# Optimization experiments

Hardware: AMD Instinct MI355X
Metric: run time of the kernel (lower is better)

Reference implementation:

```python
import jax, jax.numpy as jnp
import numpy as np

STRIDE, PAD, DIL, K = 1, 1, 1, 3  # spatial conv hyperparams (temporal kernel = 1)


def setup_inputs() -> dict:
    key = jax.random.key(0)
    k0, k1, k2, k3 = jax.random.split(key, 4)
    C_in, C_out = 256, 256
    x = jax.random.normal(k0, (2, C_in, 8, 32, 32), jnp.float32)
    # main weight keeps the dummy temporal dim of size 1, as in the torch module
    weight = jax.random.normal(k1, (C_out, C_in, 1, K, K), jnp.float32) * 0.02
    bias = jnp.zeros((C_out,), jnp.float32)
    # conv_offset: 27 = 2*9 offsets + 9 masks (3x3 kernel, 1 deformable group).
    # torch inits these to zero; use small random values so sampling is non-trivial.
    offset_w = jax.random.normal(k2, (27, C_in, 3, 3), jnp.float32) * 0.01
    offset_b = jax.random.normal(k3, (27,), jnp.float32) * 0.01
    return {"x": x, "weight": weight, "bias": bias,
            "offset_w": offset_w, "offset_b": offset_b}


def _dcn_forward(x, weight, bias, offset_w, offset_b):
    B, C, T, H, W = x.shape
    N = B * T
    # (B,C,T,H,W) -> (B*T, C, H, W)
    xf = x.transpose(0, 2, 1, 3, 4).reshape(N, C, H, W)

    # offset/mask conv (standard 3x3 conv, padding=dilation)
    om = jax.lax.conv_general_dilated(
        xf, offset_w, (STRIDE, STRIDE), [(PAD, PAD), (PAD, PAD)],
        rhs_dilation=(DIL, DIL), dimension_numbers=("NCHW", "OIHW", "NCHW"))
    om = om + offset_b[None, :, None, None]
    o1, o2, mask = jnp.split(om, 3, axis=1)              # each [N,9,Ho,Wo]
    offset = jnp.concatenate([o1, o2], axis=1)           # [N,18,Ho,Wo]
    mask = jax.nn.sigmoid(mask)
    Ho, Wo = om.shape[2], om.shape[3]
    KK = K * K

    # DCNv2 layout: interleaved (dy, dx) pairs per kernel tap
    off = offset.reshape(N, KK, 2, Ho, Wo)
    dy, dx = off[:, :, 0], off[:, :, 1]                  # [N,9,Ho,Wo]

    ki = jnp.arange(KK) // K
    kj = jnp.arange(KK) % K
    base_y = (jnp.arange(Ho) * STRIDE - PAD)[None, :] + (ki * DIL)[:, None]  # [9,Ho]
    base_x = (jnp.arange(Wo) * STRIDE - PAD)[None, :] + (kj * DIL)[:, None]  # [9,Wo]
    py = dy + base_y[None, :, :, None].astype(dy.dtype)  # [N,9,Ho,Wo]
    px = dx + base_x[None, :, None, :].astype(dx.dtype)

    y0f = jnp.floor(py); x0f = jnp.floor(px)
    ty = py - y0f; tx = px - x0f
    y0 = y0f.astype(jnp.int32); x0 = x0f.astype(jnp.int32)

    x_flat = xf.reshape(N, C, H * W)

    def gather(yy, xx, w):
        # zero padding outside image; bilinear corner weight w: [N,9,Ho,Wo]
        valid = (yy >= 0) & (yy < H) & (xx >= 0) & (xx < W)
        idx = (jnp.clip(yy, 0, H - 1) * W + jnp.clip(xx, 0, W - 1)).reshape(N, -1)
        v = jnp.take_along_axis(x_flat, idx[:, None, :], axis=2)   # [N,C,9*Ho*Wo]
        return v * (w * valid).reshape(N, 1, -1)

    val = (gather(y0,     x0,     (1 - ty) * (1 - tx))
           + gather(y0,     x0 + 1, (1 - ty) * tx)
           + gather(y0 + 1, x0,     ty * (1 - tx))
           + gather(y0 + 1, x0 + 1, ty * tx))
    val = val.reshape(N, C, KK, Ho, Wo) * mask[:, None]            # modulated samples

    w2 = weight.squeeze(2).reshape(weight.shape[0], C, KK)         # [Co,C,9]
    out = jnp.einsum('nckhw,ock->nohw', val, w2) + bias[None, :, None, None]
    # (B*T, Co, Ho, Wo) -> (B, Co, T, Ho, Wo)
    return out.reshape(B, T, -1, Ho, Wo).transpose(0, 2, 1, 3, 4)


def reference(x, weight, bias, offset_w, offset_b):
    return _dcn_forward(x, weight, bias, offset_w, offset_b)
```

## Files before the change

### kernel.cpp

```cpp
#include <hip/hip_runtime.h>
#include <math.h>

typedef __attribute__((ext_vector_type(4))) float f32x4;
typedef __attribute__((ext_vector_type(2))) float f32x2;
typedef __attribute__((ext_vector_type(8))) short s16x8;

__device__ inline unsigned f2bf(float f) {
    unsigned u = __float_as_uint(f);
    u += 0x7FFFu + ((u >> 16) & 1u);
    return u >> 16;
}
__device__ inline f32x2 unpk2(unsigned u) {
    f32x2 r;
    r.x = __uint_as_float(u << 16);
    r.y = __uint_as_float(u & 0xFFFF0000u);
    return r;
}

__global__ __launch_bounds__(256) void pack_all(const float* __restrict__ x,
                                                const float* __restrict__ w,
                                                const float* __restrict__ ow,
                                                unsigned* __restrict__ xt32,
                                                short* __restrict__ Wp,
                                                short* __restrict__ Wo)
{
    __shared__ float tile[256][33];
    const int tid = threadIdx.x;
    if (blockIdx.x < 512) {
        const int n = blockIdx.x >> 5, y = blockIdx.x & 31;
        const int b = n >> 3, ts = n & 7;
        const float* src = x + (((size_t)b * 256 * 8) + ts) * 1024 + y * 32;
        #pragma unroll
        for (int rep = 0; rep < 32; ++rep) {
            int c = rep * 8 + (tid >> 5);
            int ww = tid & 31;
            tile[c][ww] = src[(size_t)c * 8192 + ww];
        }
        __syncthreads();
        unsigned* dst = xt32 + ((size_t)n * 1024 + y * 32) * 128;
        #pragma unroll
        for (int rep = 0; rep < 16; ++rep) {
            int idx = rep * 256 + tid;
            int cp = idx & 127, ww = idx >> 7;
            unsigned lo = f2bf(tile[2 * cp][ww]);
            unsigned hi = f2bf(tile[2 * cp + 1][ww]);
            dst[(size_t)ww * 128 + cp] = lo | (hi << 16);
        }
    } else if (blockIdx.x < 768) {
        const int o = blockIdx.x - 512;
        float* lw = &tile[0][0];
        for (int k = tid; k < 2304; k += 256) lw[k] = w[(size_t)o * 2304 + k];
        __syncthreads();
        const int oq = o >> 6, mt = (o >> 4) & 3, l15 = o & 15;
        for (int idx = tid; idx < 288; idx += 256) {
            int t = idx >> 5, cb = idx & 31;
            int quad = cb & 3, kc = (cb >> 2) & 1, k2 = cb >> 3;
            int lane = quad * 16 + l15;
            union { s16x8 v; short sh[8]; } u;
            #pragma unroll
            for (int c8 = 0; c8 < 8; ++c8)
                u.sh[c8] = (short)f2bf(lw[(cb * 8 + c8) * 9 + t]);
            size_t dst = ((((size_t)(t * 4 + oq) * 4 + mt) * 4 + k2) * 2 + kc) * 512
                       + lane * 8;
            *(s16x8*)(Wp + dst) = u.v;
        }
    } else {
        const int m = blockIdx.x - 768;
        float* lw = &tile[0][0];
        if (m < 27) {
            for (int k = tid; k < 2304; k += 256) lw[k] = ow[(size_t)m * 2304 + k];
        }
        __syncthreads();
        #pragma unroll
        for (int t = 0; t < 9; ++t) {
            float v = (m < 27) ? lw[tid * 9 + t] : 0.f;
            Wo[t * 8192 + m * 256 + tid] = (short)f2bf(v);
        }
    }
}

__global__ __launch_bounds__(512) void offsets_kernel(
    const short* __restrict__ xt, const short* __restrict__ Wo,
    const float* __restrict__ ob, float4* __restrict__ descW,
    int4* __restrict__ descI)
{
    __shared__ float pom[4][32][33];
    const int tid = threadIdx.x;
    const int bs = blockIdx.x;
    const int n = bs >> 5, ho = bs & 31;
    const int lane = tid & 63, wv = tid >> 6;
    const int nt = wv & 1, kq4 = wv >> 1;
    const int l15 = lane & 15, quad = lane >> 4;
    const int pos = nt * 16 + l15;
    const short* xn = xt + (size_t)n * (1024 * 256);
    const s16x8 z8 = {0, 0, 0, 0, 0, 0, 0, 0};

    f32x4 oacc0 = {0, 0, 0, 0}, oacc1 = {0, 0, 0, 0};
    #pragma unroll
    for (int t = 0; t < 9; ++t) {
        const int ki = t / 3, kj = t - 3 * ki;
        int y = ho - 1 + ki;
        bool vy = (y >= 0) && (y < 32);
        int ycl = min(max(y, 0), 31);
        int xc = pos - 1 + kj;
        bool v = vy && (xc >= 0) && (xc < 32);
        int xcl = min(max(xc, 0), 31);
        const short* bp  = xn + (ycl * 32 + xcl) * 256;
        const short* ap0 = Wo + (t * 32 + l15) * 256;
        #pragma unroll
        for (int cc = 0; cc < 2; ++cc) {
            int c = kq4 * 64 + cc * 32 + quad * 8;
            s16x8 bfrag = *(const s16x8*)(bp + c);
            if (!v) bfrag = z8;
            s16x8 a0 = *(const s16x8*)(ap0 + c);
            s16x8 a1 = *(const s16x8*)(ap0 + 16 * 256 + c);
            oacc0 = __builtin_amdgcn_mfma_f32_16x16x32_bf16(a0, bfrag, oacc0, 0, 0, 0);
            oacc1 = __builtin_amdgcn_mfma_f32_16x16x32_bf16(a1, bfrag, oacc1, 0, 0, 0);
        }
    }
    #pragma unroll
    for (int r = 0; r < 4; ++r) {
        pom[kq4][quad * 4 + r][pos]      = oacc0[r];
        pom[kq4][16 + quad * 4 + r][pos] = oacc1[r];
    }
    __syncthreads();

    for (int s = tid; s < 288; s += 512) {
        int t = s >> 5, wo = s & 31;
        float dy = pom[0][2 * t][wo]     + pom[1][2 * t][wo]
                 + pom[2][2 * t][wo]     + pom[3][2 * t][wo]     + ob[2 * t];
        float dx = pom[0][2 * t + 1][wo] + pom[1][2 * t + 1][wo]
                 + pom[2][2 * t + 1][wo] + pom[3][2 * t + 1][wo] + ob[2 * t + 1];
        float mv = pom[0][18 + t][wo]    + pom[1][18 + t][wo]
                 + pom[2][18 + t][wo]    + pom[3][18 + t][wo]    + ob[18 + t];
        float mk = 1.0f / (1.0f + __expf(-mv));
        float py = dy + (float)(ho - 1 + t / 3);
        float px = dx + (float)(wo - 1 + t % 3);
        float y0f = floorf(py), x0f = floorf(px);
        float ty = py - y0f, tx = px - x0f;
        int y0 = (int)y0f, x0 = (int)x0f;
        int y1 = y0 + 1, x1 = x0 + 1;
        bool vy0 = (y0 >= 0) && (y0 < 32), vy1 = (y1 >= 0) && (y1 < 32);
        bool vx0 = (x0 >= 0) && (x0 < 32), vx1 = (x1 >= 0) && (x1 < 32);
        int cy0 = min(max(y0, 0), 31), cy1 = min(max(y1, 0), 31);
        int cx0 = min(max(x0, 0), 31), cx1 = min(max(x1, 0), 31);
        float b0 = (1.f - ty) * (1.f - tx) * mk * (float)(vy0 && vx0);
        float b1 = (1.f - ty) * tx         * mk * (float)(vy0 && vx1);
        float b2 = ty * (1.f - tx)         * mk * (float)(vy1 && vx0);
        float b3 = ty * tx                 * mk * (float)(vy1 && vx1);
        size_t base = (size_t)(n * 32 + ho) * 288 + s;
        descW[base] = make_float4(b0, b1, b2, b3);
        descI[base] = make_int4((cy0 * 32 + cx0) * 256, (cy0 * 32 + cx1) * 256,
                                (cy1 * 32 + cx0) * 256, (cy1 * 32 + cx1) * 256);
    }
}

template<int NK>
__global__ __launch_bounds__(256, 4) void dcn_main(
    const short* __restrict__ xt, const short* __restrict__ Wp,
    const float4* __restrict__ descW, const int4* __restrict__ descI,
    const float* __restrict__ bias, float* __restrict__ out,
    float* __restrict__ wsP)
{
    __shared__ short  sB[2][32 * 72];
    __shared__ float4 sdw[288];
    __shared__ int4   sdi[288];

    const int tid = threadIdx.x;
    constexpr int NQ = 4 / NK;
    const int bid0 = blockIdx.x;
    const int bid = (bid0 & 7) * (64 * NQ) + (bid0 >> 3);
    const int kq = bid & (NQ - 1);
    const int r  = bid / NQ;
    const int n = r >> 5, ho = r & 31;

    {
        const float4* dW = descW + (size_t)(n * 32 + ho) * 288;
        const int4*   dI = descI + (size_t)(n * 32 + ho) * 288;
        for (int i = tid; i < 288; i += 256) { sdw[i] = dW[i]; sdi[i] = dI[i]; }
    }
    __syncthreads();

    const int oct = tid & 7, pos = tid >> 3;
    const int oq = tid >> 6;
    const int lane = tid & 63, l15 = lane & 15, quad = lane >> 4;
    const short* xn = xt + (size_t)n * (1024 * 256);

    f32x4 acc[8];
    #pragma unroll
    for (int i = 0; i < 8; ++i) acc[i] = (f32x4){0, 0, 0, 0};

    uint4  g[2][4];
    float4 gw[2];

    {
        gw[0] = sdw[pos];
        const int4 i4 = sdi[pos];
        const int cc = (kq * NK) * 64 + oct * 8;
        g[0][0] = *(const uint4*)(xn + i4.x + cc);
        g[0][1] = *(const uint4*)(xn + i4.y + cc);
        g[0][2] = *(const uint4*)(xn + i4.z + cc);
        g[0][3] = *(const uint4*)(xn + i4.w + cc);
    }

    #pragma unroll
    for (int s = 0; s < 9 * NK; ++s) {
        const int cur = s & 1, nxt = cur ^ 1;
        const int t = s % 9;
        const int k2 = kq * NK + s / 9;

        s16x8 afr[4][2];
        #pragma unroll
        for (int mt = 0; mt < 4; ++mt)
            #pragma unroll
            for (int kc = 0; kc < 2; ++kc)
                afr[mt][kc] = *(const s16x8*)(Wp +
                    ((((size_t)(t * 4 + oq) * 4 + mt) * 4 + k2) * 2 + kc) * 512
                    + lane * 8);

        {
            const float4 w4 = gw[cur];
            const unsigned* p0 = (const unsigned*)&g[cur][0];
            const unsigned* p1 = (const unsigned*)&g[cur][1];
            const unsigned* p2 = (const unsigned*)&g[cur][2];
            const unsigned* p3 = (const unsigned*)&g[cur][3];
            union { s16x8 v; unsigned u[4]; } bu;
            #pragma unroll
            for (int d = 0; d < 4; ++d) {
                f32x2 a = w4.x * unpk2(p0[d]);
                a += w4.y * unpk2(p1[d]);
                a += w4.z * unpk2(p2[d]);
                a += w4.w * unpk2(p3[d]);
                asm("v_cvt_pk_bf16_f32 %0, %1, %2"
                    : "=v"(bu.u[d]) : "v"(a.x), "v"(a.y));
            }
            *(s16x8*)&sB[cur][pos * 72 + oct * 8] = bu.v;
        }

        asm volatile("s_waitcnt lgkmcnt(0)\n\ts_barrier" ::: "memory");
        __builtin_amdgcn_sched_barrier(0);

        if (s < 9 * NK - 1) {
            const int t1 = (s + 1) % 9;
            const int cb1 = (kq * NK + (s + 1) / 9) * 64;
            gw[nxt] = sdw[t1 * 32 + pos];
            const int4 i4 = sdi[t1 * 32 + pos];
            const int cc = cb1 + oct * 8;
            g[nxt][0] = *(const uint4*)(xn + i4.x + cc);
            g[nxt][1] = *(const uint4*)(xn + i4.y + cc);
            g[nxt][2] = *(const uint4*)(xn + i4.z + cc);
            g[nxt][3] = *(const uint4*)(xn + i4.w + cc);
        }

        s16x8 bfr[2][2];
        #pragma unroll
        for (int nt = 0; nt < 2; ++nt)
            #pragma unroll
            for (int kc = 0; kc < 2; ++kc)
                bfr[nt][kc] = *(const s16x8*)
                    &sB[cur][(nt * 16 + l15) * 72 + kc * 32 + quad * 8];

        #pragma unroll
        for (int mt = 0; mt < 4; ++mt)
            #pragma unroll
            for (int nt = 0; nt < 2; ++nt) {
                acc[mt * 2 + nt] = __builtin_amdgcn_mfma_f32_16x16x32_bf16(
                    afr[mt][0], bfr[nt][0], acc[mt * 2 + nt], 0, 0, 0);
                acc[mt * 2 + nt] = __builtin_amdgcn_mfma_f32_16x16x32_bf16(
                    afr[mt][1], bfr[nt][1], acc[mt * 2 + nt], 0, 0, 0);
            }
    }

    const int bb = n >> 3, ts = n & 7;
    if (kq == 0) {
        #pragma unroll
        for (int mt = 0; mt < 4; ++mt) {
            const float4 bv = *(const float4*)(bias + oq * 64 + mt * 16 + quad * 4);
            #pragma unroll
            for (int nt = 0; nt < 2; ++nt)
                #pragma unroll
                for (int rr = 0; rr < 4; ++rr) {
                    int oc = oq * 64 + mt * 16 + quad * 4 + rr;
                    int p  = nt * 16 + l15;
                    out[(((size_t)bb * 256 + oc) * 8 + ts) * 1024 + ho * 32 + p] =
                        acc[mt * 2 + nt][rr] + ((const float*)&bv)[rr];
                }
        }
    } else {
        float* wp1 = wsP + (size_t)(kq - 1) * 4194304
                         + (size_t)(n * 32 + ho) * 256 * 32;
        #pragma unroll
        for (int mt = 0; mt < 4; ++mt)
            #pragma unroll
            for (int nt = 0; nt < 2; ++nt)
                #pragma unroll
                for (int rr = 0; rr < 4; ++rr) {
                    int oc = oq * 64 + mt * 16 + quad * 4 + rr;
                    int p  = nt * 16 + l15;
                    wp1[oc * 32 + p] = acc[mt * 2 + nt][rr];
                }
    }
}

template<int NP>
__global__ __launch_bounds__(256) void reduce_out(const float* __restrict__ wsP,
                                                  float4* __restrict__ out)
{
    int i = blockIdx.x * 256 + threadIdx.x;
    int f = i * 4;
    int p  = f & 1023;
    int ts = (f >> 10) & 7;
    int oc = (f >> 13) & 255;
    int bb = f >> 21;
    int n = bb * 8 + ts;
    int ho = p >> 5, pp = p & 31;
    size_t base = ((size_t)(n * 32 + ho) * 256 + oc) * 32 + pp;
    float4 a = out[i];
    #pragma unroll
    for (int q = 0; q < NP; ++q) {
        const float4 w = *(const float4*)(wsP + (size_t)q * 4194304 + base);
        a.x += w.x; a.y += w.y; a.z += w.z; a.w += w.w;
    }
    out[i] = a;
}

extern "C" void kernel_launch(void* const* d_in, const int* in_sizes, int n_in,
                              void* d_out, int out_size, void* d_ws, size_t ws_size,
                              hipStream_t stream) {
    const float* x        = (const float*)d_in[0];
    const float* weight   = (const float*)d_in[1];
    const float* bias     = (const float*)d_in[2];
    const float* offset_w = (const float*)d_in[3];
    const float* offset_b = (const float*)d_in[4];

    char* ws = (char*)d_ws;
    short*  xt    = (short*)ws;                       ws += (size_t)16 * 1024 * 256 * 2;
    short*  Wp    = (short*)ws;                       ws += (size_t)9 * 256 * 256 * 2;
    short*  Wo    = (short*)ws;                       ws += (size_t)9 * 32 * 256 * 2;
    float4* descW = (float4*)ws;                      ws += (size_t)147456 * 16;
    int4*   descI = (int4*)ws;                        ws += (size_t)147456 * 16;
    float*  wsP   = (float*)ws;

    const bool big = ws_size >= 64765952ULL;

    pack_all      <<<800,  256, 0, stream>>>(x, weight, offset_w, (unsigned*)xt, Wp, Wo);
    offsets_kernel<<<512,  512, 0, stream>>>(xt, Wo, offset_b, descW, descI);
    if (big) {
        dcn_main<1>   <<<2048, 256, 0, stream>>>(xt, Wp, descW, descI, bias, (float*)d_out, wsP);
        reduce_out<3> <<<4096, 256, 0, stream>>>(wsP, (float4*)d_out);
    } else {
        dcn_main<2>   <<<1024, 256, 0, stream>>>(xt, Wp, descW, descI, bias, (float*)d_out, wsP);
        reduce_out<1> <<<4096, 256, 0, stream>>>(wsP, (float4*)d_out);
    }
}
```

Before: 153.0 us.

## Replace split-K DCN main kernel plus reduction with single full-K block kernel

The main deformable-conv GEMM no longer splits the 256 input channels across several blocks that write partial sums to a workspace. One 512-thread block now covers all channels for an output row, two 128-channel halves per tap, and writes the biased output directly. This drops the reduce_out kernel launch and the workspace write/read traffic. In exchange there are fewer blocks (512) for the GPU to spread over, a longer serial loop per block, and each bilinear sample is gathered only once per row.

```diff
diff --git a/kernel.cpp b/kernel.cpp
--- a/kernel.cpp
+++ b/kernel.cpp
@@ -155,40 +155,36 @@
     }
 }
 
-template<int NK>
-__global__ __launch_bounds__(256, 4) void dcn_main(
+__global__ __launch_bounds__(512, 4) void dcn_single(
     const short* __restrict__ xt, const short* __restrict__ Wp,
     const float4* __restrict__ descW, const int4* __restrict__ descI,
-    const float* __restrict__ bias, float* __restrict__ out,
-    float* __restrict__ wsP)
+    const float* __restrict__ bias, float* __restrict__ out)
 {
-    __shared__ short  sB[2][32 * 72];
+    __shared__ short  sB[2][32 * 136];
     __shared__ float4 sdw[288];
     __shared__ int4   sdi[288];
 
     const int tid = threadIdx.x;
-    constexpr int NQ = 4 / NK;
     const int bid0 = blockIdx.x;
-    const int bid = (bid0 & 7) * (64 * NQ) + (bid0 >> 3);
-    const int kq = bid & (NQ - 1);
-    const int r  = bid / NQ;
-    const int n = r >> 5, ho = r & 31;
+    const int bid = (bid0 & 7) * 64 + (bid0 >> 3);
+    const int n = bid >> 5, ho = bid & 31;
 
     {
         const float4* dW = descW + (size_t)(n * 32 + ho) * 288;
         const int4*   dI = descI + (size_t)(n * 32 + ho) * 288;
-        for (int i = tid; i < 288; i += 256) { sdw[i] = dW[i]; sdi[i] = dI[i]; }
+        for (int i = tid; i < 288; i += 512) { sdw[i] = dW[i]; sdi[i] = dI[i]; }
     }
     __syncthreads();
 
-    const int oct = tid & 7, pos = tid >> 3;
-    const int oq = tid >> 6;
+    const int oct16 = tid & 15, pos = tid >> 4;
+    const int wv = tid >> 6;
+    const int oq = wv >> 1, mtb = (wv & 1) * 2;
     const int lane = tid & 63, l15 = lane & 15, quad = lane >> 4;
     const short* xn = xt + (size_t)n * (1024 * 256);
 
-    f32x4 acc[8];
-    #pragma unroll
-    for (int i = 0; i < 8; ++i) acc[i] = (f32x4){0, 0, 0, 0};
+    f32x4 acc[4];
+    #pragma unroll
+    for (int i = 0; i < 4; ++i) acc[i] = (f32x4){0, 0, 0, 0};
 
     uint4  g[2][4];
     float4 gw[2];
@@ -196,7 +192,7 @@
     {
         gw[0] = sdw[pos];
         const int4 i4 = sdi[pos];
-        const int cc = (kq * NK) * 64 + oct * 8;
+        const int cc = oct16 * 8;
         g[0][0] = *(const uint4*)(xn + i4.x + cc);
         g[0][1] = *(const uint4*)(xn + i4.y + cc);
         g[0][2] = *(const uint4*)(xn + i4.z + cc);
@@ -204,19 +200,21 @@
     }
 
     #pragma unroll
-    for (int s = 0; s < 9 * NK; ++s) {
+    for (int s = 0; s < 18; ++s) {
         const int cur = s & 1, nxt = cur ^ 1;
         const int t = s % 9;
-        const int k2 = kq * NK + s / 9;
-
-        s16x8 afr[4][2];
-        #pragma unroll
-        for (int mt = 0; mt < 4; ++mt)
-            #pragma unroll
-            for (int kc = 0; kc < 2; ++kc)
-                afr[mt][kc] = *(const s16x8*)(Wp +
-                    ((((size_t)(t * 4 + oq) * 4 + mt) * 4 + k2) * 2 + kc) * 512
+        const int h = s / 9;
+
+        s16x8 afr[2][4];
+        #pragma unroll
+        for (int mt = 0; mt < 2; ++mt)
+            #pragma unroll
+            for (int kp = 0; kp < 4; ++kp) {
+                const int k2 = h * 2 + (kp >> 1), kc = kp & 1;
+                afr[mt][kp] = *(const s16x8*)(Wp +
+                    ((((size_t)(t * 4 + oq) * 4 + (mtb + mt)) * 4 + k2) * 2 + kc) * 512
                     + lane * 8);
+            }
 
         {
             const float4 w4 = gw[cur];
@@ -234,94 +232,56 @@
                 asm("v_cvt_pk_bf16_f32 %0, %1, %2"
                     : "=v"(bu.u[d]) : "v"(a.x), "v"(a.y));
             }
-            *(s16x8*)&sB[cur][pos * 72 + oct * 8] = bu.v;
+            *(s16x8*)&sB[cur][pos * 136 + oct16 * 8] = bu.v;
         }
 
         asm volatile("s_waitcnt lgkmcnt(0)\n\ts_barrier" ::: "memory");
         __builtin_amdgcn_sched_barrier(0);
 
-        if (s < 9 * NK - 1) {
+        if (s < 17) {
             const int t1 = (s + 1) % 9;
-            const int cb1 = (kq * NK + (s + 1) / 9) * 64;
+            const int h1 = (s + 1) / 9;
             gw[nxt] = sdw[t1 * 32 + pos];
             const int4 i4 = sdi[t1 * 32 + pos];
-            const int cc = cb1 + oct * 8;
+            const int cc = h1 * 128 + oct16 * 8;
             g[nxt][0] = *(const uint4*)(xn + i4.x + cc);
             g[nxt][1] = *(const uint4*)(xn + i4.y + cc);
             g[nxt][2] = *(const uint4*)(xn + i4.z + cc);
             g[nxt][3] = *(const uint4*)(xn + i4.w + cc);
         }
 
-        s16x8 bfr[2][2];
+        s16x8 bfr[2][4];
         #pragma unroll
         for (int nt = 0; nt < 2; ++nt)
             #pragma unroll
-            for (int kc = 0; kc < 2; ++kc)
-                bfr[nt][kc] = *(const s16x8*)
-                    &sB[cur][(nt * 16 + l15) * 72 + kc * 32 + quad * 8];
-
-        #pragma unroll
-        for (int mt = 0; mt < 4; ++mt)
-            #pragma unroll
-            for (int nt = 0; nt < 2; ++nt) {
-                acc[mt * 2 + nt] = __builtin_amdgcn_mfma_f32_16x16x32_bf16(
-                    afr[mt][0], bfr[nt][0], acc[mt * 2 + nt], 0, 0, 0);
-                acc[mt * 2 + nt] = __builtin_amdgcn_mfma_f32_16x16x32_bf16(
-                    afr[mt][1], bfr[nt][1], acc[mt * 2 + nt], 0, 0, 0);
-            }
-    }
-
-    const int bb = n >> 3, ts = n & 7;
-    if (kq == 0) {
-        #pragma unroll
-        for (int mt = 0; mt < 4; ++mt) {
-            const float4 bv = *(const float4*)(bias + oq * 64 + mt * 16 + quad * 4);
+            for (int kp = 0; kp < 4; ++kp)
+                bfr[nt][kp] = *(const s16x8*)
+                    &sB[cur][(nt * 16 + l15) * 136 + kp * 32 + quad * 8];
+
+        #pragma unroll
+        for (int mt = 0; mt < 2; ++mt)
             #pragma unroll
             for (int nt = 0; nt < 2; ++nt)
                 #pragma unroll
-                for (int rr = 0; rr < 4; ++rr) {
-                    int oc = oq * 64 + mt * 16 + quad * 4 + rr;
-                    int p  = nt * 16 + l15;
-                    out[(((size_t)bb * 256 + oc) * 8 + ts) * 1024 + ho * 32 + p] =
-                        acc[mt * 2 + nt][rr] + ((const float*)&bv)[rr];
-                }
-        }
-    } else {
-        float* wp1 = wsP + (size_t)(kq - 1) * 4194304
-                         + (size_t)(n * 32 + ho) * 256 * 32;
-        #pragma unroll
-        for (int mt = 0; mt < 4; ++mt)
-            #pragma unroll
-            for (int nt = 0; nt < 2; ++nt)
-                #pragma unroll
-                for (int rr = 0; rr < 4; ++rr) {
-                    int oc = oq * 64 + mt * 16 + quad * 4 + rr;
-                    int p  = nt * 16 + l15;
-                    wp1[oc * 32 + p] = acc[mt * 2 + nt][rr];
-                }
-    }
-}
-
-template<int NP>
-__global__ __launch_bounds__(256) void reduce_out(const float* __restrict__ wsP,
-                                                  float4* __restrict__ out)
-{
-    int i = blockIdx.x * 256 + threadIdx.x;
-    int f = i * 4;
-    int p  = f & 1023;
-    int ts = (f >> 10) & 7;
-    int oc = (f >> 13) & 255;
-    int bb = f >> 21;
-    int n = bb * 8 + ts;
-    int ho = p >> 5, pp = p & 31;
-    size_t base = ((size_t)(n * 32 + ho) * 256 + oc) * 32 + pp;
-    float4 a = out[i];
-    #pragma unroll
-    for (int q = 0; q < NP; ++q) {
-        const float4 w = *(const float4*)(wsP + (size_t)q * 4194304 + base);
-        a.x += w.x; a.y += w.y; a.z += w.z; a.w += w.w;
-    }
-    out[i] = a;
+                for (int kp = 0; kp < 4; ++kp)
+                    acc[mt * 2 + nt] = __builtin_amdgcn_mfma_f32_16x16x32_bf16(
+                        afr[mt][kp], bfr[nt][kp], acc[mt * 2 + nt], 0, 0, 0);
+    }
+
+    const int bb = n >> 3, ts = n & 7;
+    #pragma unroll
+    for (int mt = 0; mt < 2; ++mt) {
+        const float4 bv = *(const float4*)(bias + oq * 64 + (mtb + mt) * 16 + quad * 4);
+        #pragma unroll
+        for (int nt = 0; nt < 2; ++nt)
+            #pragma unroll
+            for (int rr = 0; rr < 4; ++rr) {
+                int oc = oq * 64 + (mtb + mt) * 16 + quad * 4 + rr;
+                int p  = nt * 16 + l15;
+                out[(((size_t)bb * 256 + oc) * 8 + ts) * 1024 + ho * 32 + p] =
+                    acc[mt * 2 + nt][rr] + ((const float*)&bv)[rr];
+            }
+    }
 }
 
 extern "C" void kernel_launch(void* const* d_in, const int* in_sizes, int n_in,
@@ -339,17 +299,8 @@
     short*  Wo    = (short*)ws;                       ws += (size_t)9 * 32 * 256 * 2;
     float4* descW = (float4*)ws;                      ws += (size_t)147456 * 16;
     int4*   descI = (int4*)ws;                        ws += (size_t)147456 * 16;
-    float*  wsP   = (float*)ws;
-
-    const bool big = ws_size >= 64765952ULL;
-
-    pack_all      <<<800,  256, 0, stream>>>(x, weight, offset_w, (unsigned*)xt, Wp, Wo);
-    offsets_kernel<<<512,  512, 0, stream>>>(xt, Wo, offset_b, descW, descI);
-    if (big) {
-        dcn_main<1>   <<<2048, 256, 0, stream>>>(xt, Wp, descW, descI, bias, (float*)d_out, wsP);
-        reduce_out<3> <<<4096, 256, 0, stream>>>(wsP, (float4*)d_out);
-    } else {
-        dcn_main<2>   <<<1024, 256, 0, stream>>>(xt, Wp, descW, descI, bias, (float*)d_out, wsP);
-        reduce_out<1> <<<4096, 256, 0, stream>>>(wsP, (float4*)d_out);
-    }
-}
+
+    pack_all      <<<800, 256, 0, stream>>>(x, weight, offset_w, (unsigned*)xt, Wp, Wo);
+    offsets_kernel<<<512, 512, 0, stream>>>(xt, Wo, offset_b, descW, descI);
+    dcn_single    <<<512, 512, 0, stream>>>(xt, Wp, descW, descI, bias, (float*)d_out);
+}
```

After: 142.9 us. 6.6% less time.
